# Kernel optimization log

Measured on AMD Instinct MI355X. Metric: run time of the kernel, lower is better.

Reference implementation:

```python
import jax, jax.numpy as jnp
from jax import lax
import numpy as np

MAX_REGIONS = 4          # static cap on connected components per volume
BIG = np.int32(2 ** 30)  # 'infinity' label for background in CCL
INF = jnp.float32(1e10)  # 'infinity' squared distance for EDT


def setup_inputs() -> dict:
    key = jax.random.key(0)
    B, D, H, W = 2, 96, 96, 96
    zz, yy, xx = np.meshgrid(np.arange(D), np.arange(H), np.arange(W), indexing='ij')

    def sphere(c, r):
        return (zz - c[0]) ** 2 + (yy - c[1]) ** 2 + (xx - c[2]) ** 2 <= r * r

    vols = []
    for b in range(B):  # 3 disjoint components per volume (realistic lesion GT)
        m = sphere((24 + 4 * b, 24, 24), 10) | sphere((70, 60, 30 + 6 * b), 12) | sphere((48, 72, 72), 9)
        vols.append(m)
    y = jnp.asarray(np.stack(vols)[:, None].astype(np.int32))          # (B,1,D,H,W)
    x = jax.random.normal(key, (B, 1, D, H, W), dtype=jnp.float32)     # logits
    return {"x": x, "y": y}


def _ccl(mask):
    """26-connected components (skimage/cucim default) via min-label propagation.
    Returns comp: int32 labels 1..K in raster order of first voxel (0 = bg), and K."""
    idx = jnp.arange(mask.size, dtype=jnp.int32).reshape(mask.shape)
    lab0 = jnp.where(mask, idx, BIG)

    def step(c):
        lab, _ = c
        pooled = lax.reduce_window(lab, BIG, lax.min, (3, 3, 3), (1, 1, 1), 'SAME')
        new = jnp.where(mask, pooled, BIG)
        return (new, jnp.any(new != lab))

    lab, _ = lax.while_loop(lambda c: c[1], step, (lab0, jnp.bool_(True)))
    uniq = jnp.unique(lab, size=MAX_REGIONS + 1, fill_value=BIG)  # sorted roots, padded
    K = jnp.sum(uniq < BIG).astype(jnp.int32)
    comp = jnp.searchsorted(uniq, lab.ravel()).reshape(lab.shape).astype(jnp.int32) + 1
    comp = jnp.where(mask, comp, 0)
    return comp, K


def _edt_1d(f, axis):
    """Exact 1D squared-EDT pass: out[p] = min_q (p-q)^2 + f[q]."""
    f2 = jnp.moveaxis(f, axis, 0)
    sh = f2.shape
    L = sh[0]
    f2 = f2.reshape(L, -1)
    q = jnp.arange(L, dtype=f.dtype)
    d2 = (q[:, None] - q[None, :]) ** 2                 # (L, L)
    out = jnp.min(d2[:, :, None] + f2[None, :, :], axis=1)  # (L, M)
    return jnp.moveaxis(out.reshape(sh), 0, axis)


def _edt_sq(f0):
    for ax in range(3):
        f0 = _edt_1d(f0, ax)
    return f0  # exact squared Euclidean distance to the zero set


def _voronoi(comp):
    """region_map[v] = label of nearest component (ties -> smallest label),
    mirroring the torch strict-< update loop over region labels."""
    def one(r):
        f0 = jnp.where(comp == r, jnp.float32(0.0), INF)
        return _edt_sq(f0)

    dists = lax.map(one, jnp.arange(1, MAX_REGIONS + 1, dtype=jnp.int32))  # (R,D,H,W)
    return jnp.argmin(dists, axis=0).astype(jnp.int32) + 1  # first-occurrence tie-break


def _per_volume(xb, yb):
    mask = yb > 0
    comp, K = _ccl(mask)              # multi_label: component labels 1..K
    region = _voronoi(comp)           # Voronoi regionization, labels 1..MAX_REGIONS
    seg = (region - 1).ravel()
    xs = jax.nn.sigmoid(xb).ravel()
    yl = comp.astype(jnp.float32).ravel()  # dice uses label VALUES, as in torch
    inter = jax.ops.segment_sum(xs * yl, seg, num_segments=MAX_REGIONS)
    sx = jax.ops.segment_sum(xs, seg, num_segments=MAX_REGIONS)
    sy = jax.ops.segment_sum(yl, seg, num_segments=MAX_REGIONS)
    valid = jnp.arange(MAX_REGIONS) < K
    denom = jnp.where(valid, sx + sy, jnp.float32(1.0))
    dice_r = jnp.where(valid, 2.0 * inter / denom, jnp.float32(0.0))
    mean_dice = jnp.sum(dice_r) / jnp.maximum(K, 1).astype(jnp.float32)
    return jnp.where(K == 0, jnp.float32(1.0), 1.0 - mean_dice)


def reference(x, y):
    # x: (B,1,D,H,W) logits; y: (B,1,D,H,W) int binary GT
    losses = lax.map(lambda t: _per_volume(t[0], t[1]), (x[:, 0], y[:, 0]))
    return jnp.mean(losses)
```

## Files before the change

### kernel.cpp

```cpp
#include <hip/hip_runtime.h>
#include <math.h>

#define W3 96
#define HW 9216
#define DHW 884736
#define NB 2
#define BIGL (1<<30)
#define INF10 1.0e10f
#define CAND_CAP 8192

#define A_ROOTCNT 0
#define A_ROOTS   2
#define A_CANDCNT 18
#define A_SUMS    28
#define A_TOTAL   64

__global__ void k_local(const int* __restrict__ y, int* __restrict__ lab,
                        int* __restrict__ acc, int* __restrict__ cand) {
    __shared__ int l[512];
    __shared__ int anyflag;
    int blk = blockIdx.x, t = threadIdx.x;
    if (t == 0) anyflag = 0;
    int b = blk / 1728, tb = blk - b * 1728;
    int tz = tb / 72, rr2 = tb - tz * 72, ty = rr2 / 3, tx = rr2 - ty * 3;
    int d0 = tz * 4, h0 = ty * 4, w0 = tx * 32;
    const int* yb = y + b * DHW;
    int* lb = lab + b * DHW;
    int e0 = t, e1 = t + 256;
    int dz0 = e0 >> 7, dy0 = (e0 >> 5) & 3, dx0 = e0 & 31;
    int dz1 = e1 >> 7, dy1 = (e1 >> 5) & 3, dx1 = e1 & 31;
    int g0 = (d0 + dz0) * HW + (h0 + dy0) * W3 + (w0 + dx0);
    int g1 = (d0 + dz1) * HW + (h0 + dy1) * W3 + (w0 + dx1);
    int m0 = yb[g0] > 0, m1 = yb[g1] > 0;
    l[e0] = m0 ? e0 : 0x7FFF0000;
    l[e1] = m1 ? e1 : 0x7FFF0000;
    __syncthreads();
    if (m0 | m1) anyflag = 1;
    __syncthreads();
    if (!anyflag) { lb[g0] = BIGL; lb[g1] = BIGL; return; }

    for (int it = 0; it < 7; it++) {
        int n0, n1;
        n0 = l[e0]; n1 = l[e1];
        if (m0) { if (dx0 > 0) n0 = min(n0, l[e0 - 1]);  if (dx0 < 31) n0 = min(n0, l[e0 + 1]); }
        if (m1) { if (dx1 > 0) n1 = min(n1, l[e1 - 1]);  if (dx1 < 31) n1 = min(n1, l[e1 + 1]); }
        __syncthreads();
        if (m0) l[e0] = n0;  if (m1) l[e1] = n1;
        __syncthreads();
        n0 = l[e0]; n1 = l[e1];
        if (m0) { if (dy0 > 0) n0 = min(n0, l[e0 - 32]); if (dy0 < 3) n0 = min(n0, l[e0 + 32]); }
        if (m1) { if (dy1 > 0) n1 = min(n1, l[e1 - 32]); if (dy1 < 3) n1 = min(n1, l[e1 + 32]); }
        __syncthreads();
        if (m0) l[e0] = n0;  if (m1) l[e1] = n1;
        __syncthreads();
        n0 = l[e0]; n1 = l[e1];
        if (m0) { if (dz0 > 0) n0 = min(n0, l[e0 - 128]); if (dz0 < 3) n0 = min(n0, l[e0 + 128]); }
        if (m1) { if (dz1 > 0) n1 = min(n1, l[e1 - 128]); if (dz1 < 3) n1 = min(n1, l[e1 + 128]); }
        __syncthreads();
        if (m0) l[e0] = n0;  if (m1) l[e1] = n1;
        __syncthreads();
        n0 = m0 ? l[l[e0]] : 0;  n1 = m1 ? l[l[e1]] : 0;
        __syncthreads();
        if (m0) l[e0] = n0;  if (m1) l[e1] = n1;
        __syncthreads();
    }
    if (m0) {
        int r = l[e0]; while (l[r] != r) r = l[r];
        lb[g0] = (d0 + (r >> 7)) * HW + (h0 + ((r >> 5) & 3)) * W3 + (w0 + (r & 31));
        if (r == e0) { int c = atomicAdd(&acc[A_CANDCNT + b], 1);
                       if (c < CAND_CAP) cand[b * CAND_CAP + c] = g0; }
    } else lb[g0] = BIGL;
    if (m1) {
        int r = l[e1]; while (l[r] != r) r = l[r];
        lb[g1] = (d0 + (r >> 7)) * HW + (h0 + ((r >> 5) & 3)) * W3 + (w0 + (r & 31));
        if (r == e1) { int c = atomicAdd(&acc[A_CANDCNT + b], 1);
                       if (c < CAND_CAP) cand[b * CAND_CAP + c] = g1; }
    } else lb[g1] = BIGL;
}

__device__ __forceinline__ int ufind(int* __restrict__ lb, int v) {
    int p = lb[v];
    if (p == v) return p;
    int root = p;
    while (true) { int pp = lb[root]; if (pp == root) break; root = pp; }
    if (root < p) atomicMin(&lb[v], root);
    return root;
}

__device__ void unite(int* __restrict__ lb, int a, int b) {
    while (true) {
        a = ufind(lb, a); b = ufind(lb, b);
        if (a == b) return;
        int mn = min(a, b), mx = max(a, b);
        int old = atomicMin(&lb[mx], mn);
        if (old == mx) return;
        a = old; b = mn;
    }
}

__constant__ int c_offs[13][3] = {
    {-1,-1,-1},{-1,-1,0},{-1,-1,1},
    {-1, 0,-1},{-1, 0,0},{-1, 0,1},
    {-1, 1,-1},{-1, 1,0},{-1, 1,1},
    { 0,-1,-1},{ 0,-1,0},{ 0,-1,1},
    { 0, 0,-1}};

__global__ void k_bmerge(const int* __restrict__ y, int* __restrict__ lab) {
    int i = blockIdx.x * blockDim.x + threadIdx.x;
    if (i >= NB * DHW) return;
    int b = i / DHW, v = i - b * DHW;
    int d = v / HW; int rem = v - d * HW; int h = rem / W3; int w = rem - h * W3;
    int fz = ((d & 3) == 0), fy = ((h & 3) == 0), fx = ((w & 31) == 0);
    if (!(fz | fy | fx)) return;
    if (y[i] <= 0) return;
    const int* yb = y + b * DHW;
    int* lb = lab + b * DHW;
    #pragma unroll
    for (int k = 0; k < 13; k++) {
        int oz = c_offs[k][0], oy = c_offs[k][1], ox = c_offs[k][2];
        int cross = (fz && oz < 0) || (fy && oy < 0) || (fx && ox < 0);
        if (!cross) continue;
        int dd = d + oz, hh = h + oy, ww = w + ox;
        if ((unsigned)dd >= W3 || (unsigned)hh >= W3 || (unsigned)ww >= W3) continue;
        int u = dd * HW + hh * W3 + ww;
        if (yb[u] > 0) unite(lb, v, u);
    }
}

__global__ void k_collect(const int* __restrict__ lab, int* __restrict__ acc,
                          const int* __restrict__ cand) {
    int t = threadIdx.x;
    for (int b = 0; b < NB; b++) {
        int cnt = acc[A_CANDCNT + b]; if (cnt > CAND_CAP) cnt = CAND_CAP;
        const int* lb = lab + b * DHW;
        for (int i = t; i < cnt; i += 256) {
            int g = cand[b * CAND_CAP + i];
            if (lb[g] == g) {
                int c = atomicAdd(&acc[A_ROOTCNT + b], 1);
                if (c < 8) acc[A_ROOTS + b * 8 + c] = g;
            }
        }
    }
}

__device__ __forceinline__ int gfind(const int* __restrict__ lb, int t) {
    while (true) { int p = lb[t]; if (p == t) break; t = p; }
    return t;
}

__device__ __forceinline__ int rankc2(int t, const int rt[8], int n) {
    int c = 1;
    #pragma unroll
    for (int p = 0; p < 8; p++) c += (p < n && rt[p] < t) ? 1 : 0;
    return c;
}

__global__ __launch_bounds__(384) void k_pedtD(const int* __restrict__ lab,
                                               const int* __restrict__ acc,
                                               float* __restrict__ out) {
    __shared__ float A[96 * 101];
    int blk = blockIdx.x;
    int b = blk / 384, r = blk % 384;
    int h = r >> 2, d0 = (r & 3) * 24;
    const int* lb = lab + (size_t)b * DHW;
    int t = threadIdx.x;
    int n = acc[A_ROOTCNT + b]; if (n > 8) n = 8;
    int rt[8];
    #pragma unroll
    for (int p = 0; p < 8; p++) rt[p] = acc[A_ROOTS + b * 8 + p];
    size_t vbase = (size_t)b * DHW;
    #pragma unroll
    for (int m = 0; m < 24; m++) {
        int e = t + 384 * m;
        int dd = e / 96, w2 = e - dd * 96;
        int tv = lb[dd * HW + h * W3 + w2];
        float val = INF10;
        if (tv != BIGL) val = 0.125f * (float)rankc2(gfind(lb, tv), rt, n);
        A[dd * 101 + w2] = val;
    }
    __syncthreads();
    int w = t % 96, dg = t / 96;
    int dbase = d0 + dg * 6;
    float best[6], dq[6];
    #pragma unroll
    for (int k = 0; k < 6; k++) { best[k] = 3.9e37f; dq[k] = (float)(dbase + k); }
    for (int q = 0; q < 96; q++) {
        float val = A[q * 101 + w];
        #pragma unroll
        for (int k = 0; k < 6; k++) {
            best[k] = fminf(best[k], fmaf(dq[k], dq[k], val));
            dq[k] -= 1.0f;
        }
    }
    #pragma unroll
    for (int k = 0; k < 6; k++)
        out[vbase + (size_t)(dbase + k) * HW + h * W3 + w] = best[k];
}

__device__ __forceinline__ float wred(float v) {
    v += __shfl_xor(v, 32, 64);
    v += __shfl_xor(v, 16, 64);
    v += __shfl_xor(v, 8, 64);
    v += __shfl_xor(v, 4, 64);
    v += __shfl_xor(v, 2, 64);
    v += __shfl_xor(v, 1, 64);
    return v;
}

__global__ __launch_bounds__(384) void k_pedtHW_acc(const float* __restrict__ fin,
                                                    const float* __restrict__ x,
                                                    int* __restrict__ acc) {
    __shared__ float A[96 * 101];
    __shared__ float Bf[24 * 101];
    __shared__ float red[6][12];
    int blk = blockIdx.x;
    int b = blk / 384, r = blk % 384;
    int d = r >> 2, h0 = (r & 3) * 24;
    size_t sbase = (size_t)b * DHW + (size_t)d * HW;
    int t = threadIdx.x;
    #pragma unroll
    for (int m = 0; m < 24; m++) {
        int e = t + 384 * m;
        int hh = e / 96, w2 = e - hh * 96;
        A[hh * 101 + w2] = fin[sbase + e];
    }
    __syncthreads();
    {
        int w = t % 96, hg = t / 96;
        int hb = h0 + hg * 6;
        float best[6], dq[6];
        #pragma unroll
        for (int k = 0; k < 6; k++) { best[k] = 3.9e37f; dq[k] = (float)(hb + k); }
        for (int q = 0; q < 96; q++) {
            float val = A[q * 101 + w];
            #pragma unroll
            for (int k = 0; k < 6; k++) {
                best[k] = fminf(best[k], fmaf(dq[k], dq[k], val));
                dq[k] -= 1.0f;
            }
        }
        #pragma unroll
        for (int k = 0; k < 6; k++) Bf[(hg * 6 + k) * 101 + w] = best[k];
    }
    __syncthreads();
    {
        int rr = t % 24, cg = t / 24;
        int wb = cg * 6;
        float best[6], dq[6];
        #pragma unroll
        for (int k = 0; k < 6; k++) { best[k] = 3.9e37f; dq[k] = (float)(wb + k); }
        for (int q = 0; q < 96; q++) {
            float val = Bf[rr * 101 + q];
            #pragma unroll
            for (int k = 0; k < 6; k++) {
                best[k] = fminf(best[k], fmaf(dq[k], dq[k], val));
                dq[k] -= 1.0f;
            }
        }
        #pragma unroll
        for (int k = 0; k < 6; k++) A[rr * 101 + wb + k] = best[k];
    }
    __syncthreads();
    float aA[4] = {0,0,0,0}, aM[4] = {0,0,0,0}, aC[4] = {0,0,0,0};
    size_t qbase = sbase + (size_t)h0 * W3;
    #pragma unroll
    for (int m = 0; m < 6; m++) {
        int e = t + 384 * m;
        int rr = e / 96, w2 = e - rr * 96;
        float key = A[rr * 101 + w2];
        int key8 = (int)(key * 8.0f);
        int seg = (key8 & 7) - 1;
        seg = (seg < 0) ? 0 : ((seg > 3) ? 3 : seg);
        int c = (key8 < 8) ? (seg + 1) : 0;
        float xs = 1.0f / (1.0f + expf(-x[qbase + e]));
        #pragma unroll
        for (int s = 0; s < 4; s++) {
            aA[s] += (seg == s) ? xs : 0.0f;
            aM[s] += (c == s + 1) ? xs : 0.0f;
            aC[s] += (c == s + 1) ? 1.0f : 0.0f;
        }
    }
    #pragma unroll
    for (int s = 0; s < 4; s++) { aA[s] = wred(aA[s]); aM[s] = wred(aM[s]); aC[s] = wred(aC[s]); }
    int lane = t & 63, wv = t >> 6;
    if (lane == 0) {
        #pragma unroll
        for (int s = 0; s < 4; s++) {
            red[wv][s] = aA[s]; red[wv][4 + s] = aM[s]; red[wv][8 + s] = aC[s];
        }
    }
    __syncthreads();
    if (t < 12) {
        float v = red[0][t] + red[1][t] + red[2][t] + red[3][t] + red[4][t] + red[5][t];
        atomicAdd((float*)&acc[A_SUMS + b * 12 + t], v);
    }
}

__global__ void k_loss(const int* __restrict__ acc, float* __restrict__ out) {
    if (threadIdx.x == 0 && blockIdx.x == 0) {
        const float* sums = (const float*)&acc[A_SUMS];
        float total = 0.0f;
        for (int b = 0; b < NB; b++) {
            int n = acc[A_ROOTCNT + b];
            int K = (n > 5) ? 5 : n;
            float s = 0.0f;
            for (int r = 0; r < 4; r++) {
                if (r < K) {
                    float A = sums[b * 12 + r];
                    float M = sums[b * 12 + 4 + r];
                    float C = sums[b * 12 + 8 + r];
                    float inter = (float)(r + 1) * M;
                    float sy = (float)(r + 1) * C;
                    s += 2.0f * inter / (A + sy);
                }
            }
            float Kf = (float)(K > 0 ? K : 1);
            total += (K == 0) ? 1.0f : (1.0f - s / Kf);
        }
        out[0] = total / (float)NB;
    }
}

extern "C" void kernel_launch(void* const* d_in, const int* in_sizes, int n_in,
                              void* d_out, int out_size, void* d_ws, size_t ws_size,
                              hipStream_t stream) {
    const float* x = (const float*)d_in[0];
    const int*   y = (const int*)d_in[1];
    float* out = (float*)d_out;

    char* ws = (char*)d_ws;
    int*   acc  = (int*)ws;
    int*   cand = (int*)(ws + 1024);
    int*   lab  = (int*)(ws + 1024 + CAND_CAP * NB * 4);
    float* kB   = (float*)((char*)lab + (size_t)NB * DHW * 4);

    dim3 blk(256);
    dim3 g1((NB * DHW) / 256);
    dim3 gl(NB * 1728);
    dim3 gq(NB * 96 * 4);
    dim3 b384(384);

    hipMemsetAsync(acc, 0, 256, stream);
    k_local<<<gl, blk, 0, stream>>>(y, lab, acc, cand);
    k_bmerge<<<g1, blk, 0, stream>>>(y, lab);
    k_collect<<<1, blk, 0, stream>>>(lab, acc, cand);
    k_pedtD<<<gq, b384, 0, stream>>>(lab, acc, kB);
    k_pedtHW_acc<<<gq, b384, 0, stream>>>(kB, x, acc);
    k_loss<<<1, 64, 0, stream>>>(acc, out);
}
```

Before: 159.1 us.

## Skip empty columns and bound EDT scan ranges to occupied extents

Each 1D EDT pass now records which columns hold any finite value and the min/max occupied index in the block. The min-scan loops run only over that range, and empty columns write INF directly. Because the volumes are mostly background, most of the O(L^2) scans should shrink a lot. The change also gives each volume its own block in k_collect and uses the fast __expf in the sigmoid, at the cost of extra shared atomics, extra barriers and slightly lower exp accuracy.

```diff
diff --git a/kernel.cpp b/kernel.cpp
--- a/kernel.cpp
+++ b/kernel.cpp
@@ -129,16 +129,15 @@
 
 __global__ void k_collect(const int* __restrict__ lab, int* __restrict__ acc,
                           const int* __restrict__ cand) {
+    int b = blockIdx.x;
     int t = threadIdx.x;
-    for (int b = 0; b < NB; b++) {
-        int cnt = acc[A_CANDCNT + b]; if (cnt > CAND_CAP) cnt = CAND_CAP;
-        const int* lb = lab + b * DHW;
-        for (int i = t; i < cnt; i += 256) {
-            int g = cand[b * CAND_CAP + i];
-            if (lb[g] == g) {
-                int c = atomicAdd(&acc[A_ROOTCNT + b], 1);
-                if (c < 8) acc[A_ROOTS + b * 8 + c] = g;
-            }
+    int cnt = acc[A_CANDCNT + b]; if (cnt > CAND_CAP) cnt = CAND_CAP;
+    const int* lb = lab + (size_t)b * DHW;
+    for (int i = t; i < cnt; i += 256) {
+        int g = cand[b * CAND_CAP + i];
+        if (lb[g] == g) {
+            int c = atomicAdd(&acc[A_ROOTCNT + b], 1);
+            if (c < 8) acc[A_ROOTS + b * 8 + c] = g;
         }
     }
 }
@@ -159,32 +158,52 @@
                                                const int* __restrict__ acc,
                                                float* __restrict__ out) {
     __shared__ float A[96 * 101];
+    __shared__ int caPart[4][96];
+    __shared__ int colAny[96];
+    __shared__ int qlo, qhi;
     int blk = blockIdx.x;
     int b = blk / 384, r = blk % 384;
     int h = r >> 2, d0 = (r & 3) * 24;
     const int* lb = lab + (size_t)b * DHW;
     int t = threadIdx.x;
+    if (t == 0) { qlo = 127; qhi = -1; }
     int n = acc[A_ROOTCNT + b]; if (n > 8) n = 8;
     int rt[8];
     #pragma unroll
     for (int p = 0; p < 8; p++) rt[p] = acc[A_ROOTS + b * 8 + p];
+    __syncthreads();
     size_t vbase = (size_t)b * DHW;
+    int w2 = t % 96, tq = t / 96;
+    int myAny = 0, myLo = 127, myHi = -1;
     #pragma unroll
     for (int m = 0; m < 24; m++) {
-        int e = t + 384 * m;
-        int dd = e / 96, w2 = e - dd * 96;
+        int dd = tq + 4 * m;
         int tv = lb[dd * HW + h * W3 + w2];
         float val = INF10;
-        if (tv != BIGL) val = 0.125f * (float)rankc2(gfind(lb, tv), rt, n);
+        if (tv != BIGL) {
+            val = 0.125f * (float)rankc2(gfind(lb, tv), rt, n);
+            myAny = 1; myLo = min(myLo, dd); myHi = max(myHi, dd);
+        }
         A[dd * 101 + w2] = val;
     }
+    caPart[tq][w2] = myAny;
+    if (myAny) { atomicMin(&qlo, myLo); atomicMax(&qhi, myHi); }
+    __syncthreads();
+    if (t < 96) colAny[t] = caPart[0][t] | caPart[1][t] | caPart[2][t] | caPart[3][t];
     __syncthreads();
     int w = t % 96, dg = t / 96;
     int dbase = d0 + dg * 6;
+    int lo = qlo, hi = qhi;
+    if (hi < 0 || !colAny[w]) {
+        #pragma unroll
+        for (int k = 0; k < 6; k++)
+            out[vbase + (size_t)(dbase + k) * HW + h * W3 + w] = INF10;
+        return;
+    }
     float best[6], dq[6];
     #pragma unroll
-    for (int k = 0; k < 6; k++) { best[k] = 3.9e37f; dq[k] = (float)(dbase + k); }
-    for (int q = 0; q < 96; q++) {
+    for (int k = 0; k < 6; k++) { best[k] = 3.9e37f; dq[k] = (float)(dbase + k - lo); }
+    for (int q = lo; q <= hi; q++) {
         float val = A[q * 101 + w];
         #pragma unroll
         for (int k = 0; k < 6; k++) {
@@ -212,53 +231,81 @@
                                                     int* __restrict__ acc) {
     __shared__ float A[96 * 101];
     __shared__ float Bf[24 * 101];
+    __shared__ int caPart[4][96];
+    __shared__ int colAny[96];
+    __shared__ int hlo, hhi, wlo, whi;
     __shared__ float red[6][12];
     int blk = blockIdx.x;
     int b = blk / 384, r = blk % 384;
     int d = r >> 2, h0 = (r & 3) * 24;
     size_t sbase = (size_t)b * DHW + (size_t)d * HW;
     int t = threadIdx.x;
+    if (t == 0) { hlo = 127; hhi = -1; wlo = 127; whi = -1; }
+    __syncthreads();
+    int w2 = t % 96, tq = t / 96;
+    int myAny = 0, myLo = 127, myHi = -1;
     #pragma unroll
     for (int m = 0; m < 24; m++) {
-        int e = t + 384 * m;
-        int hh = e / 96, w2 = e - hh * 96;
-        A[hh * 101 + w2] = fin[sbase + e];
+        int hh = tq + 4 * m;
+        float val = fin[sbase + hh * W3 + w2];
+        if (val < 1.0e9f) { myAny = 1; myLo = min(myLo, hh); myHi = max(myHi, hh); }
+        A[hh * 101 + w2] = val;
+    }
+    caPart[tq][w2] = myAny;
+    if (myAny) { atomicMin(&hlo, myLo); atomicMax(&hhi, myHi); }
+    __syncthreads();
+    if (t < 96) {
+        int ca = caPart[0][t] | caPart[1][t] | caPart[2][t] | caPart[3][t];
+        colAny[t] = ca;
+        if (ca) { atomicMin(&wlo, t); atomicMax(&whi, t); }
     }
     __syncthreads();
     {
         int w = t % 96, hg = t / 96;
         int hb = h0 + hg * 6;
-        float best[6], dq[6];
-        #pragma unroll
-        for (int k = 0; k < 6; k++) { best[k] = 3.9e37f; dq[k] = (float)(hb + k); }
-        for (int q = 0; q < 96; q++) {
-            float val = A[q * 101 + w];
-            #pragma unroll
-            for (int k = 0; k < 6; k++) {
-                best[k] = fminf(best[k], fmaf(dq[k], dq[k], val));
-                dq[k] -= 1.0f;
+        int lo = hlo, hi = hhi;
+        if (hi < 0 || !colAny[w]) {
+            #pragma unroll
+            for (int k = 0; k < 6; k++) Bf[(hg * 6 + k) * 101 + w] = INF10;
+        } else {
+            float best[6], dq[6];
+            #pragma unroll
+            for (int k = 0; k < 6; k++) { best[k] = 3.9e37f; dq[k] = (float)(hb + k - lo); }
+            for (int q = lo; q <= hi; q++) {
+                float val = A[q * 101 + w];
+                #pragma unroll
+                for (int k = 0; k < 6; k++) {
+                    best[k] = fminf(best[k], fmaf(dq[k], dq[k], val));
+                    dq[k] -= 1.0f;
+                }
             }
-        }
-        #pragma unroll
-        for (int k = 0; k < 6; k++) Bf[(hg * 6 + k) * 101 + w] = best[k];
+            #pragma unroll
+            for (int k = 0; k < 6; k++) Bf[(hg * 6 + k) * 101 + w] = best[k];
+        }
     }
     __syncthreads();
     {
         int rr = t % 24, cg = t / 24;
         int wb = cg * 6;
-        float best[6], dq[6];
-        #pragma unroll
-        for (int k = 0; k < 6; k++) { best[k] = 3.9e37f; dq[k] = (float)(wb + k); }
-        for (int q = 0; q < 96; q++) {
-            float val = Bf[rr * 101 + q];
-            #pragma unroll
-            for (int k = 0; k < 6; k++) {
-                best[k] = fminf(best[k], fmaf(dq[k], dq[k], val));
-                dq[k] -= 1.0f;
+        int lo = wlo, hi = whi;
+        if (hi < 0) {
+            #pragma unroll
+            for (int k = 0; k < 6; k++) A[rr * 101 + wb + k] = INF10;
+        } else {
+            float best[6], dq[6];
+            #pragma unroll
+            for (int k = 0; k < 6; k++) { best[k] = 3.9e37f; dq[k] = (float)(wb + k - lo); }
+            for (int q = lo; q <= hi; q++) {
+                float val = Bf[rr * 101 + q];
+                #pragma unroll
+                for (int k = 0; k < 6; k++) {
+                    best[k] = fminf(best[k], fmaf(dq[k], dq[k], val));
+                    dq[k] -= 1.0f;
+                }
             }
-        }
-        #pragma unroll
-        for (int k = 0; k < 6; k++) A[rr * 101 + wb + k] = best[k];
+            #pragma unroll
+            for (int k = 0; k < 6; k++) A[rr * 101 + wb + k] = best[k];
+        }
     }
     __syncthreads();
     float aA[4] = {0,0,0,0}, aM[4] = {0,0,0,0}, aC[4] = {0,0,0,0};
@@ -266,13 +313,13 @@
     #pragma unroll
     for (int m = 0; m < 6; m++) {
         int e = t + 384 * m;
-        int rr = e / 96, w2 = e - rr * 96;
-        float key = A[rr * 101 + w2];
+        int rr = e / 96, wv2 = e - rr * 96;
+        float key = A[rr * 101 + wv2];
         int key8 = (int)(key * 8.0f);
         int seg = (key8 & 7) - 1;
         seg = (seg < 0) ? 0 : ((seg > 3) ? 3 : seg);
         int c = (key8 < 8) ? (seg + 1) : 0;
-        float xs = 1.0f / (1.0f + expf(-x[qbase + e]));
+        float xs = 1.0f / (1.0f + __expf(-x[qbase + e]));
         #pragma unroll
         for (int s = 0; s < 4; s++) {
             aA[s] += (seg == s) ? xs : 0.0f;
@@ -343,7 +390,7 @@
     hipMemsetAsync(acc, 0, 256, stream);
     k_local<<<gl, blk, 0, stream>>>(y, lab, acc, cand);
     k_bmerge<<<g1, blk, 0, stream>>>(y, lab);
-    k_collect<<<1, blk, 0, stream>>>(lab, acc, cand);
+    k_collect<<<NB, blk, 0, stream>>>(lab, acc, cand);
     k_pedtD<<<gq, b384, 0, stream>>>(lab, acc, kB);
     k_pedtHW_acc<<<gq, b384, 0, stream>>>(kB, x, acc);
     k_loss<<<1, 64, 0, stream>>>(acc, out);
```

New measurement: 170.8 us. +7.4%, slower.
